# Kernel tuning notes

Hardware: AMD Instinct MI355X
Metric: run time of the kernel (lower is better)

## Reference

```python
import jax, jax.numpy as jnp
import numpy as np

BLOCK = (16, 16)  # (block rows over out_features, block cols over in_features)
TOKENS, IN_F, OUT_F = 8192, 4096, 4096


def setup_inputs() -> dict:
    key = jax.random.key(0)
    k1, k2, k3, k4 = jax.random.split(key, 4)
    x = jax.random.normal(k1, (TOKENS, IN_F), dtype=jnp.float32)
    weight = jax.random.normal(k2, (OUT_F, IN_F), dtype=jnp.float32) / np.sqrt(IN_F)
    bias = jax.random.normal(k3, (OUT_F,), dtype=jnp.float32)
    block_mask = jax.random.bernoulli(k4, 0.5, (OUT_F // BLOCK[0], IN_F // BLOCK[1]))
    return {"x": x, "weight": weight, "bias": bias, "block_mask": block_mask}


def _expand_mask(block_mask, dtype):
    # [X, Y] block mask -> [out_features, in_features] dense 0/1 mask
    m = jnp.repeat(block_mask, BLOCK[0], axis=0)
    m = jnp.repeat(m, BLOCK[1], axis=1)
    return m.astype(dtype)


def reference(x, weight, bias, block_mask):
    # Sparse path: block-sparse matmul with the block-masked weight
    # (blocksparseMM(sparse_data, x, block_size) == x @ (W * mask).T)
    w_sparse = weight * _expand_mask(block_mask, weight.dtype)
    x_sparse = jnp.einsum('ti,oi->to', x, w_sparse)
    # Dense residual path: standard linear with the full weight + bias
    x_dense = jnp.einsum('ti,oi->to', x, weight) + bias
    return x_sparse + x_dense
```

## Files before the change

### kernel.cpp

```cpp
#include <hip/hip_runtime.h>
#include <hip/hip_bf16.h>
#include <stdint.h>

#define TOKENS 8192
#define IN_F   4096
#define OUT_F  4096

typedef __attribute__((ext_vector_type(4))) float  f32x4;
typedef __attribute__((ext_vector_type(8))) __bf16 bf16x8;

__device__ __forceinline__ unsigned short f2bf(float f) {
    union { float f; uint32_t u; } c; c.f = f;
    uint32_t u = c.u;
    u += 0x7fffu + ((u >> 16) & 1);
    return (unsigned short)(u >> 16);
}

__device__ __forceinline__ void load_lds_16(const void* gptr, void* lptr) {
    __builtin_amdgcn_global_load_lds(
        (const __attribute__((address_space(1))) unsigned int*)gptr,
        (__attribute__((address_space(3))) unsigned int*)lptr, 16, 0, 0);
}

template<int N> __device__ __forceinline__ void vm_bar() {
    if constexpr (N == 4) asm volatile("s_waitcnt vmcnt(4)\ns_barrier" ::: "memory");
    else                  asm volatile("s_waitcnt vmcnt(0)\ns_barrier" ::: "memory");
}
__device__ __forceinline__ void bar() { asm volatile("s_barrier" ::: "memory"); }

#define XBLOCKS 2048
#define WBLOCKS 1024
__global__ __launch_bounds__(256) void cvt_kernel(const float* __restrict__ x,
                                                  const float* __restrict__ w,
                                                  const int* __restrict__ mask,
                                                  unsigned short* __restrict__ xb,
                                                  unsigned short* __restrict__ wb) {
    int b = blockIdx.x;
    if (b < XBLOCKS) {
        const int n4 = TOKENS * IN_F / 4;
        int i = b * 256 + threadIdx.x;
        const int stride = XBLOCKS * 256;
        for (; i < n4; i += stride) {
            float4 v = ((const float4*)x)[i];
            ushort4 o;
            o.x = f2bf(v.x); o.y = f2bf(v.y); o.z = f2bf(v.z); o.w = f2bf(v.w);
            ((ushort4*)xb)[i] = o;
        }
    } else {
        const int n4 = OUT_F * IN_F / 4;
        int i = (b - XBLOCKS) * 256 + threadIdx.x;
        const int stride = WBLOCKS * 256;
        for (; i < n4; i += stride) {
            int elem = i * 4;
            int o = elem >> 12;
            int k = elem & (IN_F - 1);
            int mb = mask[(o >> 4) * (IN_F / 16) + (k >> 4)];
            float s = mb ? 2.0f : 1.0f;
            float4 v = ((const float4*)w)[i];
            ushort4 ov;
            ov.x = f2bf(v.x * s); ov.y = f2bf(v.y * s);
            ov.z = f2bf(v.z * s); ov.w = f2bf(v.w * s);
            ((ushort4*)wb)[i] = ov;
        }
    }
}

#define BM 256
#define BN 256
#define BK 64
#define NT (IN_F / BK)

#define ST_A(T, H) {                                                           \
    const unsigned short* s_ = srcA + (size_t)(T) * BK + (H) * 32;             \
    unsigned short* d_ = sm + (((T) & 1) * 16384 + (H) * 8192) + dstL;         \
    load_lds_16(s_, d_);                                                       \
    load_lds_16(s_ + (size_t)128 * IN_F, d_ + 4096); }
#define ST_B(T, H) {                                                           \
    const unsigned short* s_ = srcB + (size_t)(T) * BK + (H) * 32;             \
    unsigned short* d_ = sm + (32768 + ((T) & 1) * 16384 + (H) * 8192) + dstL; \
    load_lds_16(s_, d_);                                                       \
    load_lds_16(s_ + (size_t)128 * IN_F, d_ + 4096); }

#define RD_B4(BUF, KS) {                                                       \
    const unsigned short* p_ = sm + 32768 + (BUF) * 16384 + (KS) * 8192 + b_base; \
    bb0 = *(const bf16x8*)(p_);        bb1 = *(const bf16x8*)(p_ + 512);       \
    bb2 = *(const bf16x8*)(p_ + 1024); bb3 = *(const bf16x8*)(p_ + 1536); }

#define RD_A4(BUF, KS, MH) {                                                   \
    const unsigned short* p_ = sm + (BUF) * 16384 + (KS) * 8192 + (MH) * 2048 + a_base; \
    aa0 = *(const bf16x8*)(p_);        aa1 = *(const bf16x8*)(p_ + 512);       \
    aa2 = *(const bf16x8*)(p_ + 1024); aa3 = *(const bf16x8*)(p_ + 1536); }

#define MM16(MH) {                                                             \
    __builtin_amdgcn_s_setprio(1);                                             \
    acc[(MH)*4+0][0] = __builtin_amdgcn_mfma_f32_16x16x32_bf16(aa0, bb0, acc[(MH)*4+0][0], 0, 0, 0); \
    acc[(MH)*4+0][1] = __builtin_amdgcn_mfma_f32_16x16x32_bf16(aa0, bb1, acc[(MH)*4+0][1], 0, 0, 0); \
    acc[(MH)*4+0][2] = __builtin_amdgcn_mfma_f32_16x16x32_bf16(aa0, bb2, acc[(MH)*4+0][2], 0, 0, 0); \
    acc[(MH)*4+0][3] = __builtin_amdgcn_mfma_f32_16x16x32_bf16(aa0, bb3, acc[(MH)*4+0][3], 0, 0, 0); \
    acc[(MH)*4+1][0] = __builtin_amdgcn_mfma_f32_16x16x32_bf16(aa1, bb0, acc[(MH)*4+1][0], 0, 0, 0); \
    acc[(MH)*4+1][1] = __builtin_amdgcn_mfma_f32_16x16x32_bf16(aa1, bb1, acc[(MH)*4+1][1], 0, 0, 0); \
    acc[(MH)*4+1][2] = __builtin_amdgcn_mfma_f32_16x16x32_bf16(aa1, bb2, acc[(MH)*4+1][2], 0, 0, 0); \
    acc[(MH)*4+1][3] = __builtin_amdgcn_mfma_f32_16x16x32_bf16(aa1, bb3, acc[(MH)*4+1][3], 0, 0, 0); \
    acc[(MH)*4+2][0] = __builtin_amdgcn_mfma_f32_16x16x32_bf16(aa2, bb0, acc[(MH)*4+2][0], 0, 0, 0); \
    acc[(MH)*4+2][1] = __builtin_amdgcn_mfma_f32_16x16x32_bf16(aa2, bb1, acc[(MH)*4+2][1], 0, 0, 0); \
    acc[(MH)*4+2][2] = __builtin_amdgcn_mfma_f32_16x16x32_bf16(aa2, bb2, acc[(MH)*4+2][2], 0, 0, 0); \
    acc[(MH)*4+2][3] = __builtin_amdgcn_mfma_f32_16x16x32_bf16(aa2, bb3, acc[(MH)*4+2][3], 0, 0, 0); \
    acc[(MH)*4+3][0] = __builtin_amdgcn_mfma_f32_16x16x32_bf16(aa3, bb0, acc[(MH)*4+3][0], 0, 0, 0); \
    acc[(MH)*4+3][1] = __builtin_amdgcn_mfma_f32_16x16x32_bf16(aa3, bb1, acc[(MH)*4+3][1], 0, 0, 0); \
    acc[(MH)*4+3][2] = __builtin_amdgcn_mfma_f32_16x16x32_bf16(aa3, bb2, acc[(MH)*4+3][2], 0, 0, 0); \
    acc[(MH)*4+3][3] = __builtin_amdgcn_mfma_f32_16x16x32_bf16(aa3, bb3, acc[(MH)*4+3][3], 0, 0, 0); \
    __builtin_amdgcn_s_setprio(0); }

#define KTILE(STG, LAST, BC, TN)                                               \
  {                                                                            \
    vm_bar<4>();                                                               \
    if (STG) ST_A(TN, 0)                                                       \
    RD_B4(BC, 0) RD_A4(BC, 0, 0)                                               \
    MM16(0)                                                                    \
    bar();                                                                     \
    if (STG) ST_B(TN, 0)                                                       \
    RD_A4(BC, 0, 1)                                                            \
    MM16(1)                                                                    \
    if (LAST) { vm_bar<0>(); } else { vm_bar<4>(); }                           \
    if (STG) ST_A(TN, 1)                                                       \
    RD_B4(BC, 1) RD_A4(BC, 1, 0)                                               \
    MM16(0)                                                                    \
    bar();                                                                     \
    if (STG) ST_B(TN, 1)                                                       \
    RD_A4(BC, 1, 1)                                                            \
    MM16(1)                                                                    \
  }

__global__ __launch_bounds__(512, 2) void gemm8_kernel(const unsigned short* __restrict__ A,
                                                       const unsigned short* __restrict__ B,
                                                       const float* __restrict__ bias,
                                                       float* __restrict__ C) {
    extern __shared__ __align__(16) unsigned short sm[];

    const int tid  = threadIdx.x;
    const int lane = tid & 63;
    const int wid  = tid >> 6;
    const int wr   = wid >> 2;
    const int wc   = wid & 3;

    const int nwg = (TOKENS / BM) * (OUT_F / BN);
    int bid = blockIdx.x;
    int swz = (bid & 7) * (nwg >> 3) + (bid >> 3);
    const int tiles_n = OUT_F / BN;
    const int t0 = (swz / tiles_n) * BM;
    const int o0 = (swz % tiles_n) * BN;

    const int srow = tid >> 2;
    const int sc   = tid & 3;
    const int scs  = sc ^ ((srow >> 1) & 3);
    const unsigned short* srcA = A + (size_t)(t0 + srow) * IN_F + scs * 8;
    const unsigned short* srcB = B + (size_t)(o0 + srow) * IN_F + scs * 8;
    const int dstL = srow * 32 + sc * 8;

    const int l15 = lane & 15, q = lane >> 4;
    const int qe = q ^ ((l15 >> 1) & 3);
    const int a_base = (wr * 128 + l15) * 32 + qe * 8;
    const int b_base = (wc * 64 + l15) * 32 + qe * 8;

    f32x4 acc[8][4];
#pragma unroll
    for (int i = 0; i < 8; ++i)
#pragma unroll
        for (int j = 0; j < 4; ++j) acc[i][j] = (f32x4)0.0f;

    bf16x8 aa0, aa1, aa2, aa3, bb0, bb1, bb2, bb3;

    ST_A(0, 0) ST_B(0, 0) ST_A(0, 1) ST_B(0, 1)

#pragma unroll 1
    for (int T = 0; T < NT - 1; ++T) {
        const int bc = T & 1;
        KTILE(true, false, bc, T + 1)
    }
    {   const int bc = (NT - 1) & 1;
        KTILE(false, true, bc, 0)
    }

    float bv[4];
#pragma unroll
    for (int nf = 0; nf < 4; ++nf) bv[nf] = bias[o0 + wc * 64 + nf * 16 + l15];
#pragma unroll
    for (int mf = 0; mf < 8; ++mf) {
        const int t = t0 + wr * 128 + mf * 16 + q * 4;
#pragma unroll
        for (int nf = 0; nf < 4; ++nf) {
            const int o = o0 + wc * 64 + nf * 16 + l15;
#pragma unroll
            for (int r = 0; r < 4; ++r)
                C[(size_t)(t + r) * OUT_F + o] = acc[mf][nf][r] + bv[nf];
        }
    }
}

__global__ __launch_bounds__(256) void gemm_f32_fallback(const float* __restrict__ x,
                                                         const float* __restrict__ w,
                                                         const float* __restrict__ bias,
                                                         const int* __restrict__ mask,
                                                         float* __restrict__ out) {
    __shared__ float As[64][17];
    __shared__ float Bs[64][17];
    int bid = blockIdx.x;
    const int tiles_n = OUT_F / 64;
    int tm = bid / tiles_n, tn = bid % tiles_n;
    int t0 = tm * 64, o0 = tn * 64;
    int tid = threadIdx.x;
    int tx = tid & 15, ty = tid >> 4;
    int lrow = tid >> 2, lc4 = (tid & 3) * 4;
    float acc[4][4] = {};
    for (int k0 = 0; k0 < IN_F; k0 += 16) {
        float4 av = *(const float4*)&x[(size_t)(t0 + lrow) * IN_F + k0 + lc4];
        float4 bv = *(const float4*)&w[(size_t)(o0 + lrow) * IN_F + k0 + lc4];
        int mb = mask[((o0 + lrow) >> 4) * (IN_F / 16) + ((k0 + lc4) >> 4)];
        float s = mb ? 2.0f : 1.0f;
        As[lrow][lc4 + 0] = av.x; As[lrow][lc4 + 1] = av.y;
        As[lrow][lc4 + 2] = av.z; As[lrow][lc4 + 3] = av.w;
        Bs[lrow][lc4 + 0] = bv.x * s; Bs[lrow][lc4 + 1] = bv.y * s;
        Bs[lrow][lc4 + 2] = bv.z * s; Bs[lrow][lc4 + 3] = bv.w * s;
        __syncthreads();
#pragma unroll
        for (int kk = 0; kk < 16; ++kk) {
            float av2[4], bv2[4];
#pragma unroll
            for (int i = 0; i < 4; ++i) av2[i] = As[ty * 4 + i][kk];
#pragma unroll
            for (int j = 0; j < 4; ++j) bv2[j] = Bs[tx * 4 + j][kk];
#pragma unroll
            for (int i = 0; i < 4; ++i)
#pragma unroll
                for (int j = 0; j < 4; ++j) acc[i][j] += av2[i] * bv2[j];
        }
        __syncthreads();
    }
#pragma unroll
    for (int j = 0; j < 4; ++j) {
        int o = o0 + tx * 4 + j;
        float bv = bias[o];
#pragma unroll
        for (int i = 0; i < 4; ++i)
            out[(size_t)(t0 + ty * 4 + i) * OUT_F + o] = acc[i][j] + bv;
    }
}

extern "C" void kernel_launch(void* const* d_in, const int* in_sizes, int n_in,
                              void* d_out, int out_size, void* d_ws, size_t ws_size,
                              hipStream_t stream) {
    const float* x    = (const float*)d_in[0];
    const float* wgt  = (const float*)d_in[1];
    const float* bias = (const float*)d_in[2];
    const int*   mask = (const int*)d_in[3];
    float* out = (float*)d_out;

    size_t xb_bytes = (size_t)TOKENS * IN_F * 2;
    size_t wb_bytes = (size_t)OUT_F * IN_F * 2;

    if (ws_size >= xb_bytes + wb_bytes) {
        unsigned short* xb = (unsigned short*)d_ws;
        unsigned short* wb = (unsigned short*)((char*)d_ws + xb_bytes);
        hipLaunchKernelGGL(cvt_kernel, dim3(XBLOCKS + WBLOCKS), dim3(256), 0, stream,
                           x, wgt, mask, xb, wb);
        (void)hipFuncSetAttribute((const void*)gemm8_kernel,
                                  hipFuncAttributeMaxDynamicSharedMemorySize, 131072);
        hipLaunchKernelGGL(gemm8_kernel, dim3((TOKENS / BM) * (OUT_F / BN)), dim3(512),
                           131072, stream, xb, wb, bias, out);
    } else {
        hipLaunchKernelGGL(gemm_f32_fallback, dim3((TOKENS / 64) * (OUT_F / 64)), dim3(256), 0, stream,
                           x, wgt, bias, mask, out);
    }
}
```

Baseline: 291.5 us.

## Software-pipeline LDS fragment reads with double-buffered registers in GEMM loop

The main K-loop of the bf16 GEMM is restructured so LDS reads for the next MFMA group go into a second set of A/B fragment registers while the current group's MFMAs run. Explicit lgkmcnt waits with scheduling barriers replace the plain s_barrier calls, and the first fragments are loaded before the loop starts. The aim is to hide LDS read latency behind matrix-core work and to drop some workgroup barriers. In exchange it needs 32 extra VGPRs per thread, which risks spilling under the 512x2 launch bound, and it depends on tightly hand-set wait counts for correctness.

```diff
diff --git a/kernel.cpp b/kernel.cpp
--- a/kernel.cpp
+++ b/kernel.cpp
@@ -26,7 +26,12 @@
     if constexpr (N == 4) asm volatile("s_waitcnt vmcnt(4)\ns_barrier" ::: "memory");
     else                  asm volatile("s_waitcnt vmcnt(0)\ns_barrier" ::: "memory");
 }
-__device__ __forceinline__ void bar() { asm volatile("s_barrier" ::: "memory"); }
+template<int N> __device__ __forceinline__ void lgkm() {
+    if constexpr (N == 8)      asm volatile("s_waitcnt lgkmcnt(8)" ::: "memory");
+    else if constexpr (N == 4) asm volatile("s_waitcnt lgkmcnt(4)" ::: "memory");
+    else                       asm volatile("s_waitcnt lgkmcnt(0)" ::: "memory");
+    __builtin_amdgcn_sched_barrier(0);
+}
 
 #define XBLOCKS 2048
 #define WBLOCKS 1024
@@ -81,55 +86,35 @@
     load_lds_16(s_, d_);                                                       \
     load_lds_16(s_ + (size_t)128 * IN_F, d_ + 4096); }
 
-#define RD_B4(BUF, KS) {                                                       \
+#define RDB4(R0, R1, R2, R3, BUF, KS) {                                        \
     const unsigned short* p_ = sm + 32768 + (BUF) * 16384 + (KS) * 8192 + b_base; \
-    bb0 = *(const bf16x8*)(p_);        bb1 = *(const bf16x8*)(p_ + 512);       \
-    bb2 = *(const bf16x8*)(p_ + 1024); bb3 = *(const bf16x8*)(p_ + 1536); }
-
-#define RD_A4(BUF, KS, MH) {                                                   \
+    R0 = *(const bf16x8*)(p_);        R1 = *(const bf16x8*)(p_ + 512);         \
+    R2 = *(const bf16x8*)(p_ + 1024); R3 = *(const bf16x8*)(p_ + 1536); }
+
+#define RDA4(R0, R1, R2, R3, BUF, KS, MH) {                                    \
     const unsigned short* p_ = sm + (BUF) * 16384 + (KS) * 8192 + (MH) * 2048 + a_base; \
-    aa0 = *(const bf16x8*)(p_);        aa1 = *(const bf16x8*)(p_ + 512);       \
-    aa2 = *(const bf16x8*)(p_ + 1024); aa3 = *(const bf16x8*)(p_ + 1536); }
-
-#define MM16(MH) {                                                             \
+    R0 = *(const bf16x8*)(p_);        R1 = *(const bf16x8*)(p_ + 512);         \
+    R2 = *(const bf16x8*)(p_ + 1024); R3 = *(const bf16x8*)(p_ + 1536); }
+
+#define MM16(A0, A1, A2, A3, B0, B1, B2, B3, MH) {                             \
     __builtin_amdgcn_s_setprio(1);                                             \
-    acc[(MH)*4+0][0] = __builtin_amdgcn_mfma_f32_16x16x32_bf16(aa0, bb0, acc[(MH)*4+0][0], 0, 0, 0); \
-    acc[(MH)*4+0][1] = __builtin_amdgcn_mfma_f32_16x16x32_bf16(aa0, bb1, acc[(MH)*4+0][1], 0, 0, 0); \
-    acc[(MH)*4+0][2] = __builtin_amdgcn_mfma_f32_16x16x32_bf16(aa0, bb2, acc[(MH)*4+0][2], 0, 0, 0); \
-    acc[(MH)*4+0][3] = __builtin_amdgcn_mfma_f32_16x16x32_bf16(aa0, bb3, acc[(MH)*4+0][3], 0, 0, 0); \
-    acc[(MH)*4+1][0] = __builtin_amdgcn_mfma_f32_16x16x32_bf16(aa1, bb0, acc[(MH)*4+1][0], 0, 0, 0); \
-    acc[(MH)*4+1][1] = __builtin_amdgcn_mfma_f32_16x16x32_bf16(aa1, bb1, acc[(MH)*4+1][1], 0, 0, 0); \
-    acc[(MH)*4+1][2] = __builtin_amdgcn_mfma_f32_16x16x32_bf16(aa1, bb2, acc[(MH)*4+1][2], 0, 0, 0); \
-    acc[(MH)*4+1][3] = __builtin_amdgcn_mfma_f32_16x16x32_bf16(aa1, bb3, acc[(MH)*4+1][3], 0, 0, 0); \
-    acc[(MH)*4+2][0] = __builtin_amdgcn_mfma_f32_16x16x32_bf16(aa2, bb0, acc[(MH)*4+2][0], 0, 0, 0); \
-    acc[(MH)*4+2][1] = __builtin_amdgcn_mfma_f32_16x16x32_bf16(aa2, bb1, acc[(MH)*4+2][1], 0, 0, 0); \
-    acc[(MH)*4+2][2] = __builtin_amdgcn_mfma_f32_16x16x32_bf16(aa2, bb2, acc[(MH)*4+2][2], 0, 0, 0); \
-    acc[(MH)*4+2][3] = __builtin_amdgcn_mfma_f32_16x16x32_bf16(aa2, bb3, acc[(MH)*4+2][3], 0, 0, 0); \
-    acc[(MH)*4+3][0] = __builtin_amdgcn_mfma_f32_16x16x32_bf16(aa3, bb0, acc[(MH)*4+3][0], 0, 0, 0); \
-    acc[(MH)*4+3][1] = __builtin_amdgcn_mfma_f32_16x16x32_bf16(aa3, bb1, acc[(MH)*4+3][1], 0, 0, 0); \
-    acc[(MH)*4+3][2] = __builtin_amdgcn_mfma_f32_16x16x32_bf16(aa3, bb2, acc[(MH)*4+3][2], 0, 0, 0); \
-    acc[(MH)*4+3][3] = __builtin_amdgcn_mfma_f32_16x16x32_bf16(aa3, bb3, acc[(MH)*4+3][3], 0, 0, 0); \
+    acc[(MH)*4+0][0] = __builtin_amdgcn_mfma_f32_16x16x32_bf16(A0, B0, acc[(MH)*4+0][0], 0, 0, 0); \
+    acc[(MH)*4+0][1] = __builtin_amdgcn_mfma_f32_16x16x32_bf16(A0, B1, acc[(MH)*4+0][1], 0, 0, 0); \
+    acc[(MH)*4+0][2] = __builtin_amdgcn_mfma_f32_16x16x32_bf16(A0, B2, acc[(MH)*4+0][2], 0, 0, 0); \
+    acc[(MH)*4+0][3] = __builtin_amdgcn_mfma_f32_16x16x32_bf16(A0, B3, acc[(MH)*4+0][3], 0, 0, 0); \
+    acc[(MH)*4+1][0] = __builtin_amdgcn_mfma_f32_16x16x32_bf16(A1, B0, acc[(MH)*4+1][0], 0, 0, 0); \
+    acc[(MH)*4+1][1] = __builtin_amdgcn_mfma_f32_16x16x32_bf16(A1, B1, acc[(MH)*4+1][1], 0, 0, 0); \
+    acc[(MH)*4+1][2] = __builtin_amdgcn_mfma_f32_16x16x32_bf16(A1, B2, acc[(MH)*4+1][2], 0, 0, 0); \
+    acc[(MH)*4+1][3] = __builtin_amdgcn_mfma_f32_16x16x32_bf16(A1, B3, acc[(MH)*4+1][3], 0, 0, 0); \
+    acc[(MH)*4+2][0] = __builtin_amdgcn_mfma_f32_16x16x32_bf16(A2, B0, acc[(MH)*4+2][0], 0, 0, 0); \
+    acc[(MH)*4+2][1] = __builtin_amdgcn_mfma_f32_16x16x32_bf16(A2, B1, acc[(MH)*4+2][1], 0, 0, 0); \
+    acc[(MH)*4+2][2] = __builtin_amdgcn_mfma_f32_16x16x32_bf16(A2, B2, acc[(MH)*4+2][2], 0, 0, 0); \
+    acc[(MH)*4+2][3] = __builtin_amdgcn_mfma_f32_16x16x32_bf16(A2, B3, acc[(MH)*4+2][3], 0, 0, 0); \
+    acc[(MH)*4+3][0] = __builtin_amdgcn_mfma_f32_16x16x32_bf16(A3, B0, acc[(MH)*4+3][0], 0, 0, 0); \
+    acc[(MH)*4+3][1] = __builtin_amdgcn_mfma_f32_16x16x32_bf16(A3, B1, acc[(MH)*4+3][1], 0, 0, 0); \
+    acc[(MH)*4+3][2] = __builtin_amdgcn_mfma_f32_16x16x32_bf16(A3, B2, acc[(MH)*4+3][2], 0, 0, 0); \
+    acc[(MH)*4+3][3] = __builtin_amdgcn_mfma_f32_16x16x32_bf16(A3, B3, acc[(MH)*4+3][3], 0, 0, 0); \
     __builtin_amdgcn_s_setprio(0); }
-
-#define KTILE(STG, LAST, BC, TN)                                               \
-  {                                                                            \
-    vm_bar<4>();                                                               \
-    if (STG) ST_A(TN, 0)                                                       \
-    RD_B4(BC, 0) RD_A4(BC, 0, 0)                                               \
-    MM16(0)                                                                    \
-    bar();                                                                     \
-    if (STG) ST_B(TN, 0)                                                       \
-    RD_A4(BC, 0, 1)                                                            \
-    MM16(1)                                                                    \
-    if (LAST) { vm_bar<0>(); } else { vm_bar<4>(); }                           \
-    if (STG) ST_A(TN, 1)                                                       \
-    RD_B4(BC, 1) RD_A4(BC, 1, 0)                                               \
-    MM16(0)                                                                    \
-    bar();                                                                     \
-    if (STG) ST_B(TN, 1)                                                       \
-    RD_A4(BC, 1, 1)                                                            \
-    MM16(1)                                                                    \
-  }
 
 __global__ __launch_bounds__(512, 2) void gemm8_kernel(const unsigned short* __restrict__ A,
                                                        const unsigned short* __restrict__ B,
@@ -168,17 +153,52 @@
 #pragma unroll
         for (int j = 0; j < 4; ++j) acc[i][j] = (f32x4)0.0f;
 
-    bf16x8 aa0, aa1, aa2, aa3, bb0, bb1, bb2, bb3;
+    bf16x8 aaE0, aaE1, aaE2, aaE3, aaO0, aaO1, aaO2, aaO3;
+    bf16x8 bbE0, bbE1, bbE2, bbE3, bbO0, bbO1, bbO2, bbO3;
 
     ST_A(0, 0) ST_B(0, 0) ST_A(0, 1) ST_B(0, 1)
+    vm_bar<4>();
+    RDB4(bbE0, bbE1, bbE2, bbE3, 0, 0)
+    RDA4(aaE0, aaE1, aaE2, aaE3, 0, 0, 0)
 
 #pragma unroll 1
     for (int T = 0; T < NT - 1; ++T) {
-        const int bc = T & 1;
-        KTILE(true, false, bc, T + 1)
-    }
-    {   const int bc = (NT - 1) & 1;
-        KTILE(false, true, bc, 0)
+        const int bc = T & 1, nbc = bc ^ 1;
+        ST_A(T + 1, 0)
+        RDA4(aaO0, aaO1, aaO2, aaO3, bc, 0, 1)
+        lgkm<4>();
+        MM16(aaE0, aaE1, aaE2, aaE3, bbE0, bbE1, bbE2, bbE3, 0)
+        ST_B(T + 1, 0)
+        vm_bar<4>();
+        RDB4(bbO0, bbO1, bbO2, bbO3, bc, 1)
+        RDA4(aaE0, aaE1, aaE2, aaE3, bc, 1, 0)
+        lgkm<8>();
+        MM16(aaO0, aaO1, aaO2, aaO3, bbE0, bbE1, bbE2, bbE3, 1)
+        ST_A(T + 1, 1)
+        RDA4(aaO0, aaO1, aaO2, aaO3, bc, 1, 1)
+        lgkm<4>();
+        MM16(aaE0, aaE1, aaE2, aaE3, bbO0, bbO1, bbO2, bbO3, 0)
+        ST_B(T + 1, 1)
+        vm_bar<4>();
+        RDB4(bbE0, bbE1, bbE2, bbE3, nbc, 0)
+        RDA4(aaE0, aaE1, aaE2, aaE3, nbc, 0, 0)
+        lgkm<8>();
+        MM16(aaO0, aaO1, aaO2, aaO3, bbO0, bbO1, bbO2, bbO3, 1)
+    }
+    {
+        RDA4(aaO0, aaO1, aaO2, aaO3, 1, 0, 1)
+        lgkm<4>();
+        MM16(aaE0, aaE1, aaE2, aaE3, bbE0, bbE1, bbE2, bbE3, 0)
+        vm_bar<0>();
+        RDB4(bbO0, bbO1, bbO2, bbO3, 1, 1)
+        RDA4(aaE0, aaE1, aaE2, aaE3, 1, 1, 0)
+        lgkm<8>();
+        MM16(aaO0, aaO1, aaO2, aaO3, bbE0, bbE1, bbE2, bbE3, 1)
+        RDA4(aaO0, aaO1, aaO2, aaO3, 1, 1, 1)
+        lgkm<4>();
+        MM16(aaE0, aaE1, aaE2, aaE3, bbO0, bbO1, bbO2, bbO3, 0)
+        lgkm<0>();
+        MM16(aaO0, aaO1, aaO2, aaO3, bbO0, bbO1, bbO2, bbO3, 1)
     }
 
     float bv[4];
```

Measured after the change: 288.8 us. No clear change (-0.9%).
